# Optimization experiments

Hardware: AMD Instinct MI355X
Metric: run time of the kernel (lower is better)

The kernel has to match this reference:

```python
import jax, jax.numpy as jnp
import numpy as np

NUM_HEADS = 16

def setup_inputs() -> dict:
    key = jax.random.key(0)
    k0, k1, k2, k3 = jax.random.split(key, 4)
    B, N, Nl, Nr, D = 16, 257, 514, 512, 1024
    gather_idx = jax.random.randint(k0, (B, N), 0, B * Nl + Nr, dtype=jnp.int64 if jax.config.jax_enable_x64 else jnp.int32)
    lhs_states = jax.random.normal(k1, (4, B, Nl, D), dtype=jnp.float32)
    rhs_states = jax.random.normal(k2, (4, 1, Nr, D), dtype=jnp.float32)
    Wo = jax.random.normal(k3, (D, D), dtype=jnp.float32) * 0.02
    bo = jnp.zeros((D,), dtype=jnp.float32)
    return {"gather_idx": gather_idx, "lhs_states": lhs_states, "rhs_states": rhs_states, "Wo": Wo, "bo": bo}


def _gather_stacked_batched_states(gather_idx, lhs_states, rhs_states):
    # lhs_states: [4, B, Nl, D] cache; rhs_states: [4, 1, Nr, D]
    # torch builds batched_states [4, 1, B*Nl+Nr, D] then gathers with [4, B, N, D] idx
    S, B, Nl, D = lhs_states.shape
    Nr = rhs_states.shape[2]
    batched = jnp.concatenate(
        [lhs_states.reshape(S, B * Nl, D), rhs_states.reshape(S, Nr, D)], axis=1
    )  # [4, B*Nl+Nr, D]
    N = gather_idx.shape[1]
    gathered = jnp.take(batched, gather_idx.reshape(-1), axis=1)  # [4, B*N, D]
    return gathered.reshape(S, B, N, D)


def reference(gather_idx, lhs_states, rhs_states, Wo, bo):
    # Gather hidden/q/k/v states from the expanded cache buffer (token reuse dispatch)
    gathered = _gather_stacked_batched_states(gather_idx, lhs_states, rhs_states)
    hidden, q, k, v = gathered[0], gathered[1], gathered[2], gathered[3]
    B, N, D = hidden.shape
    H = NUM_HEADS
    hd = D // H
    scale = hd ** -0.5
    # _shape: [B, N, D] -> [B, H, N, hd]; query scaled before bmm as in torch
    qh = (q * scale).reshape(B, N, H, hd).transpose(0, 2, 1, 3)
    kh = k.reshape(B, N, H, hd).transpose(0, 2, 1, 3)
    vh = v.reshape(B, N, H, hd).transpose(0, 2, 1, 3)
    attn_weights = jax.nn.softmax(jnp.einsum('bhqd,bhkd->bhqk', qh, kh), axis=-1)
    attn_out = jnp.einsum('bhqk,bhkd->bhqd', attn_weights, vh)  # [B, H, N, hd]
    attn_out = attn_out.transpose(0, 2, 1, 3).reshape(B, N, D)
    attn_out = attn_out @ Wo.T + bo  # out_proj (torch Linear)
    return hidden + attn_out  # residual
```

## Files before the change

### kernel.cpp

```cpp
#include <hip/hip_runtime.h>
#include <hip/hip_bf16.h>

typedef __attribute__((ext_vector_type(8))) short bf16x8;
typedef __attribute__((ext_vector_type(4))) float f32x4;
typedef unsigned short u16;
typedef unsigned int u32;

#define LHS_STRIDE 8421376
#define RHS_STRIDE 524288
#define TBL_SPLIT  8224
#define AN 257
#define KSD 68
#define VSD 292
#define PSD 292

__device__ __forceinline__ const float* tbl_row(int s, int g,
    const float* __restrict__ lhs, const float* __restrict__ rhs) {
  if (g < TBL_SPLIT) return lhs + (size_t)s * LHS_STRIDE + (size_t)g * 1024;
  return rhs + (size_t)s * RHS_STRIDE + (size_t)(g - TBL_SPLIT) * 1024;
}

__device__ __forceinline__ u16 f2b(float x) {
  union { __hip_bfloat16 b; u16 u; } c;
  c.b = __float2bfloat16(x);
  return c.u;
}

__device__ __forceinline__ bf16x8 mk8(ushort4 a, ushort4 b) {
  bf16x8 r;
  r[0] = (short)a.x; r[1] = (short)a.y; r[2] = (short)a.z; r[3] = (short)a.w;
  r[4] = (short)b.x; r[5] = (short)b.y; r[6] = (short)b.z; r[7] = (short)b.w;
  return r;
}

__device__ __forceinline__ void gload16(const u16* g, u16* l) {
  __builtin_amdgcn_global_load_lds((const __attribute__((address_space(1))) void*)g,
                                   (__attribute__((address_space(3))) void*)l,
                                   16, 0, 0);
}

struct __align__(16) AttnSmem {
  int idx[260];
  u16 K[272 * KSD];
  u16 VT[64 * VSD];
  u16 P[8 * 16 * PSD];
};

__global__ __launch_bounds__(512, 1) void attn_kernel(
    const int* __restrict__ gidx, const float* __restrict__ lhs,
    const float* __restrict__ rhs, u16* __restrict__ attn_out) {
  __shared__ AttnSmem sm;
  const int bh = blockIdx.x, b = bh >> 4, h = bh & 15;
  const int t = threadIdx.x, wave = t >> 6, lane = t & 63;
  const int lg = lane >> 4, lr = lane & 15;

  {
    uint4 z = {0u, 0u, 0u, 0u};
    uint4* p = (uint4*)sm.VT;
    const int n16 = (64 * VSD + 8 * 16 * PSD) * 2 / 16;
    for (int i = t; i < n16; i += 512) p[i] = z;
  }
  for (int i = t; i < AN; i += 512) sm.idx[i] = gidx[b * AN + i];
  __syncthreads();

  {
    const int sr = t >> 4, c4 = (t & 15) * 4;
    for (int pass = 0; pass < 9; ++pass) {
      int r = pass * 32 + sr;
      if (r < AN) {
        int g = sm.idx[r];
        float4 kv = *(const float4*)(tbl_row(2, g, lhs, rhs) + h * 64 + c4);
        *(ushort4*)&sm.K[r * KSD + c4] =
            make_ushort4(f2b(kv.x), f2b(kv.y), f2b(kv.z), f2b(kv.w));
        float4 vv = *(const float4*)(tbl_row(3, g, lhs, rhs) + h * 64 + c4);
        sm.VT[(c4 + 0) * VSD + r] = f2b(vv.x);
        sm.VT[(c4 + 1) * VSD + r] = f2b(vv.y);
        sm.VT[(c4 + 2) * VSD + r] = f2b(vv.z);
        sm.VT[(c4 + 3) * VSD + r] = f2b(vv.w);
      }
    }
  }
  __syncthreads();

  u16* Pw = sm.P + wave * 16 * PSD;
  for (int rt = wave; rt < 17; rt += 8) {
    const int r0 = rt * 16;

    bf16x8 qa[2];
    {
      int qrow = r0 + lr;
      int g = sm.idx[qrow < AN ? qrow : 0];
      const float* qp = tbl_row(1, g, lhs, rhs) + h * 64 + lg * 8;
#pragma unroll
      for (int kf = 0; kf < 2; ++kf) {
        float4 v0 = *(const float4*)(qp + kf * 32);
        float4 v1 = *(const float4*)(qp + kf * 32 + 4);
        bf16x8 a;
        a[0] = (short)f2b(0.125f * v0.x); a[1] = (short)f2b(0.125f * v0.y);
        a[2] = (short)f2b(0.125f * v0.z); a[3] = (short)f2b(0.125f * v0.w);
        a[4] = (short)f2b(0.125f * v1.x); a[5] = (short)f2b(0.125f * v1.y);
        a[6] = (short)f2b(0.125f * v1.z); a[7] = (short)f2b(0.125f * v1.w);
        qa[kf] = a;
      }
    }

    f32x4 s[17];
#pragma unroll
    for (int nf = 0; nf < 17; ++nf) {
      const u16* kp = &sm.K[(nf * 16 + lr) * KSD + lg * 8];
      ushort4 x0 = *(const ushort4*)kp;
      ushort4 x1 = *(const ushort4*)(kp + 4);
      ushort4 y0 = *(const ushort4*)(kp + 32);
      ushort4 y1 = *(const ushort4*)(kp + 36);
      f32x4 acc = {0.f, 0.f, 0.f, 0.f};
      acc = __builtin_amdgcn_mfma_f32_16x16x32_bf16(qa[0], mk8(x0, x1), acc, 0, 0, 0);
      acc = __builtin_amdgcn_mfma_f32_16x16x32_bf16(qa[1], mk8(y0, y1), acc, 0, 0, 0);
      s[nf] = acc;
    }
    if (lr != 0) { s[16][0] = -1e30f; s[16][1] = -1e30f; s[16][2] = -1e30f; s[16][3] = -1e30f; }

    float inv[4];
#pragma unroll
    for (int reg = 0; reg < 4; ++reg) {
      float m = -1e30f;
#pragma unroll
      for (int nf = 0; nf < 17; ++nf) m = fmaxf(m, s[nf][reg]);
#pragma unroll
      for (int off = 1; off < 16; off <<= 1) m = fmaxf(m, __shfl_xor(m, off, 16));
      float sum = 0.f;
#pragma unroll
      for (int nf = 0; nf < 17; ++nf) {
        float w = __expf(s[nf][reg] - m);
        s[nf][reg] = w;
        sum += w;
      }
#pragma unroll
      for (int off = 1; off < 16; off <<= 1) sum += __shfl_xor(sum, off, 16);
      inv[reg] = 1.0f / sum;
    }
#pragma unroll
    for (int reg = 0; reg < 4; ++reg) {
#pragma unroll
      for (int nf = 0; nf < 17; ++nf)
        Pw[(lg * 4 + reg) * PSD + nf * 16 + lr] = f2b(s[nf][reg] * inv[reg]);
    }

    f32x4 zero = {0.f, 0.f, 0.f, 0.f};
    f32x4 o[4] = {zero, zero, zero, zero};
#pragma unroll
    for (int ks = 0; ks < 9; ++ks) {
      const u16* pp = &Pw[lr * PSD + ks * 32 + lg * 8];
      bf16x8 pa = mk8(*(const ushort4*)pp, *(const ushort4*)(pp + 4));
#pragma unroll
      for (int nd = 0; nd < 4; ++nd) {
        const u16* vp = &sm.VT[(nd * 16 + lr) * VSD + ks * 32 + lg * 8];
        bf16x8 vb = mk8(*(const ushort4*)vp, *(const ushort4*)(vp + 4));
        o[nd] = __builtin_amdgcn_mfma_f32_16x16x32_bf16(pa, vb, o[nd], 0, 0, 0);
      }
    }

#pragma unroll
    for (int nd = 0; nd < 4; ++nd)
#pragma unroll
      for (int reg = 0; reg < 4; ++reg) {
        int row = r0 + lg * 4 + reg;
        if (row < AN)
          attn_out[(size_t)(b * AN + row) * 1024 + h * 64 + nd * 16 + lr] =
              f2b(o[nd][reg]);
      }
  }
}

__global__ void cvt_wo_kernel(const float* __restrict__ w, u16* __restrict__ o) {
  int i = blockIdx.x * 256 + threadIdx.x;
  float4 v = ((const float4*)w)[i];
  ((ushort4*)o)[i] = make_ushort4(f2b(v.x), f2b(v.y), f2b(v.z), f2b(v.w));
}

__global__ __launch_bounds__(256, 1) void gemm_kernel(
    const u16* __restrict__ A, const u16* __restrict__ Bw,
    const float* __restrict__ bo, const int* __restrict__ gidx,
    const float* __restrict__ lhs, const float* __restrict__ rhs,
    float* __restrict__ out) {
  __shared__ __align__(16) u16 As[128 * 32];
  __shared__ __align__(16) u16 Bs[128 * 32];
  const int t = threadIdx.x, wave = t >> 6, lane = t & 63;
  const int lg = lane >> 4, lr = lane & 15;
  const int mt = blockIdx.x >> 3, nt = blockIdx.x & 7;
  const int m0 = mt * 128, n0 = nt * 128;
  const int wm = wave >> 1, wn = wave & 1;

  f32x4 zero = {0.f, 0.f, 0.f, 0.f};
  f32x4 acc[4][4];
#pragma unroll
  for (int i = 0; i < 4; ++i)
#pragma unroll
    for (int j = 0; j < 4; ++j) acc[i][j] = zero;

  const int srow = lane >> 2;
  const int scol = (((lane & 3) ^ ((lane >> 3) & 3))) * 8;
  const int ss = (lg ^ ((lr >> 1) & 3)) * 8;

  for (int kt = 0; kt < 32; ++kt) {
    const int k0 = kt * 32;
#pragma unroll
    for (int i = 0; i < 2; ++i) {
      int row = wave * 32 + i * 16 + srow;
      int arow = m0 + row; if (arow > 4111) arow = 4111;
      gload16(A + (size_t)arow * 1024 + k0 + scol, &As[wave * 1024 + i * 512]);
      gload16(Bw + (size_t)(n0 + row) * 1024 + k0 + scol, &Bs[wave * 1024 + i * 512]);
    }
    __syncthreads();
    bf16x8 af[4], bfr[4];
#pragma unroll
    for (int i = 0; i < 4; ++i) {
      af[i]  = *(const bf16x8*)&As[(wm * 64 + i * 16 + lr) * 32 + ss];
      bfr[i] = *(const bf16x8*)&Bs[(wn * 64 + i * 16 + lr) * 32 + ss];
    }
#pragma unroll
    for (int i = 0; i < 4; ++i)
#pragma unroll
      for (int j = 0; j < 4; ++j)
        acc[i][j] = __builtin_amdgcn_mfma_f32_16x16x32_bf16(af[i], bfr[j], acc[i][j], 0, 0, 0);
    __syncthreads();
  }

#pragma unroll
  for (int i = 0; i < 4; ++i)
#pragma unroll
    for (int j = 0; j < 4; ++j)
#pragma unroll
      for (int reg = 0; reg < 4; ++reg) {
        int row = m0 + wm * 64 + i * 16 + lg * 4 + reg;
        int col = n0 + wn * 64 + j * 16 + lr;
        if (row < 4112) {
          int g = gidx[row];
          out[(size_t)row * 1024 + col] =
              tbl_row(0, g, lhs, rhs)[col] + bo[col] + acc[i][j][reg];
        }
      }
}

extern "C" void kernel_launch(void* const* d_in, const int* in_sizes, int n_in,
                              void* d_out, int out_size, void* d_ws, size_t ws_size,
                              hipStream_t stream) {
  const int*   gidx = (const int*)d_in[0];
  const float* lhs  = (const float*)d_in[1];
  const float* rhs  = (const float*)d_in[2];
  const float* Wo   = (const float*)d_in[3];
  const float* bo   = (const float*)d_in[4];
  float* out = (float*)d_out;

  u16* attn_ws = (u16*)d_ws;
  u16* wo_bf   = attn_ws + (size_t)4112 * 1024;

  cvt_wo_kernel<<<1024, 256, 0, stream>>>(Wo, wo_bf);
  attn_kernel<<<256, 512, 0, stream>>>(gidx, lhs, rhs, attn_ws);
  gemm_kernel<<<264, 256, 0, stream>>>(attn_ws, wo_bf, bo, gidx, lhs, rhs, out);
}
```

Baseline: 262.9 us.

## Fuse Wo conversion into attention, keep P in registers, double-buffer GEMM

Folds the Wo fp32-to-bf16 conversion into the attention kernel, which saves a launch. The attention kernel now prefetches K/V/Q into registers before writing shared memory. It drops the shared P buffer and the zero-init pass: QK^T is computed transposed so softmax is done per column, and the P fragments are rebuilt with cross-lane shuffles. The last key column gets its own MFMA, and occupancy is raised to 2 blocks per CU. The GEMM gets double-buffered LDS staging so global loads overlap compute, at the cost of more registers and LDS.

After: 302.2 us. 14.9% more time.

```diff
diff --git a/kernel.cpp b/kernel.cpp
--- a/kernel.cpp
+++ b/kernel.cpp
@@ -11,8 +11,7 @@
 #define TBL_SPLIT  8224
 #define AN 257
 #define KSD 68
-#define VSD 292
-#define PSD 292
+#define VSD 260
 
 __device__ __forceinline__ const float* tbl_row(int s, int g,
     const float* __restrict__ lhs, const float* __restrict__ rhs) {
@@ -24,6 +23,10 @@
   union { __hip_bfloat16 b; u16 u; } c;
   c.b = __float2bfloat16(x);
   return c.u;
+}
+
+__device__ __forceinline__ u32 pk2(float a, float b) {
+  return (u32)f2b(a) | ((u32)f2b(b) << 16);
 }
 
 __device__ __forceinline__ bf16x8 mk8(ushort4 a, ushort4 b) {
@@ -40,56 +43,39 @@
 }
 
 struct __align__(16) AttnSmem {
-  int idx[260];
   u16 K[272 * KSD];
   u16 VT[64 * VSD];
-  u16 P[8 * 16 * PSD];
 };
 
-__global__ __launch_bounds__(512, 1) void attn_kernel(
+__global__ __launch_bounds__(512, 2) void attn_kernel(
     const int* __restrict__ gidx, const float* __restrict__ lhs,
-    const float* __restrict__ rhs, u16* __restrict__ attn_out) {
+    const float* __restrict__ rhs, u16* __restrict__ attn_out,
+    const float* __restrict__ Wo, u16* __restrict__ wo_bf) {
   __shared__ AttnSmem sm;
   const int bh = blockIdx.x, b = bh >> 4, h = bh & 15;
   const int t = threadIdx.x, wave = t >> 6, lane = t & 63;
   const int lg = lane >> 4, lr = lane & 15;
-
-  {
-    uint4 z = {0u, 0u, 0u, 0u};
-    uint4* p = (uint4*)sm.VT;
-    const int n16 = (64 * VSD + 8 * 16 * PSD) * 2 / 16;
-    for (int i = t; i < n16; i += 512) p[i] = z;
-  }
-  for (int i = t; i < AN; i += 512) sm.idx[i] = gidx[b * AN + i];
-  __syncthreads();
-
-  {
-    const int sr = t >> 4, c4 = (t & 15) * 4;
-    for (int pass = 0; pass < 9; ++pass) {
-      int r = pass * 32 + sr;
-      if (r < AN) {
-        int g = sm.idx[r];
-        float4 kv = *(const float4*)(tbl_row(2, g, lhs, rhs) + h * 64 + c4);
-        *(ushort4*)&sm.K[r * KSD + c4] =
-            make_ushort4(f2b(kv.x), f2b(kv.y), f2b(kv.z), f2b(kv.w));
-        float4 vv = *(const float4*)(tbl_row(3, g, lhs, rhs) + h * 64 + c4);
-        sm.VT[(c4 + 0) * VSD + r] = f2b(vv.x);
-        sm.VT[(c4 + 1) * VSD + r] = f2b(vv.y);
-        sm.VT[(c4 + 2) * VSD + r] = f2b(vv.z);
-        sm.VT[(c4 + 3) * VSD + r] = f2b(vv.w);
-      }
-    }
-  }
-  __syncthreads();
-
-  u16* Pw = sm.P + wave * 16 * PSD;
-  for (int rt = wave; rt < 17; rt += 8) {
-    const int r0 = rt * 16;
-
-    bf16x8 qa[2];
-    {
-      int qrow = r0 + lr;
-      int g = sm.idx[qrow < AN ? qrow : 0];
+  const int* gi = gidx + b * AN;
+
+  const int sr = t >> 4, c4v = (t & 15) * 4;
+  float4 kreg[9], vreg[9];
+#pragma unroll
+  for (int p = 0; p < 9; ++p) {
+    int r = p * 32 + sr;
+    int rc = (r < AN) ? r : 0;
+    int g = gi[rc];
+    kreg[p] = *(const float4*)(tbl_row(2, g, lhs, rhs) + h * 64 + c4v);
+    vreg[p] = *(const float4*)(tbl_row(3, g, lhs, rhs) + h * 64 + c4v);
+  }
+
+  const int ntile = (wave == 0) ? 3 : 2;
+  const int rts[3] = {wave, wave + 8, 16};
+  bf16x8 qa[3][2];
+#pragma unroll
+  for (int ti = 0; ti < 3; ++ti) {
+    if (ti < ntile) {
+      int qrow = rts[ti] * 16 + lr; if (qrow > 256) qrow = 256;
+      int g = gi[qrow];
       const float* qp = tbl_row(1, g, lhs, rhs) + h * 64 + lg * 8;
 #pragma unroll
       for (int kf = 0; kf < 2; ++kf) {
@@ -100,9 +86,42 @@
         a[2] = (short)f2b(0.125f * v0.z); a[3] = (short)f2b(0.125f * v0.w);
         a[4] = (short)f2b(0.125f * v1.x); a[5] = (short)f2b(0.125f * v1.y);
         a[6] = (short)f2b(0.125f * v1.z); a[7] = (short)f2b(0.125f * v1.w);
-        qa[kf] = a;
-      }
-    }
+        qa[ti][kf] = a;
+      }
+    }
+  }
+
+  {
+    const float4* src = (const float4*)Wo;
+    ushort4* dst = (ushort4*)wo_bf;
+    int i0 = bh * 1024 + t * 2;
+#pragma unroll
+    for (int u = 0; u < 2; ++u) {
+      float4 v = src[i0 + u];
+      dst[i0 + u] = make_ushort4(f2b(v.x), f2b(v.y), f2b(v.z), f2b(v.w));
+    }
+  }
+
+#pragma unroll
+  for (int p = 0; p < 9; ++p) {
+    int r = p * 32 + sr;
+    if (r < AN) {
+      *(ushort4*)&sm.K[r * KSD + c4v] =
+          make_ushort4(f2b(kreg[p].x), f2b(kreg[p].y), f2b(kreg[p].z), f2b(kreg[p].w));
+      sm.VT[(c4v + 0) * VSD + r] = f2b(vreg[p].x);
+      sm.VT[(c4v + 1) * VSD + r] = f2b(vreg[p].y);
+      sm.VT[(c4v + 2) * VSD + r] = f2b(vreg[p].z);
+      sm.VT[(c4v + 3) * VSD + r] = f2b(vreg[p].w);
+    }
+  }
+  __syncthreads();
+
+  const int srcE = lr + ((lane & 16) << 1);
+  const int srcO = srcE + 16;
+  const bool useE = (lg < 2);
+
+  for (int ti = 0; ti < ntile; ++ti) {
+    const int r0 = rts[ti] * 16;
 
     f32x4 s[17];
 #pragma unroll
@@ -113,49 +132,65 @@
       ushort4 y0 = *(const ushort4*)(kp + 32);
       ushort4 y1 = *(const ushort4*)(kp + 36);
       f32x4 acc = {0.f, 0.f, 0.f, 0.f};
-      acc = __builtin_amdgcn_mfma_f32_16x16x32_bf16(qa[0], mk8(x0, x1), acc, 0, 0, 0);
-      acc = __builtin_amdgcn_mfma_f32_16x16x32_bf16(qa[1], mk8(y0, y1), acc, 0, 0, 0);
+      acc = __builtin_amdgcn_mfma_f32_16x16x32_bf16(mk8(x0, x1), qa[ti][0], acc, 0, 0, 0);
+      acc = __builtin_amdgcn_mfma_f32_16x16x32_bf16(mk8(y0, y1), qa[ti][1], acc, 0, 0, 0);
       s[nf] = acc;
     }
-    if (lr != 0) { s[16][0] = -1e30f; s[16][1] = -1e30f; s[16][2] = -1e30f; s[16][3] = -1e30f; }
-
-    float inv[4];
-#pragma unroll
-    for (int reg = 0; reg < 4; ++reg) {
-      float m = -1e30f;
-#pragma unroll
-      for (int nf = 0; nf < 17; ++nf) m = fmaxf(m, s[nf][reg]);
-#pragma unroll
-      for (int off = 1; off < 16; off <<= 1) m = fmaxf(m, __shfl_xor(m, off, 16));
-      float sum = 0.f;
-#pragma unroll
-      for (int nf = 0; nf < 17; ++nf) {
-        float w = __expf(s[nf][reg] - m);
-        s[nf][reg] = w;
+    s[16][1] = -1e30f; s[16][2] = -1e30f; s[16][3] = -1e30f;
+    if (lg != 0) s[16][0] = -1e30f;
+
+    float m = -1e30f;
+#pragma unroll
+    for (int nf = 0; nf < 17; ++nf)
+      m = fmaxf(m, fmaxf(fmaxf(s[nf][0], s[nf][1]), fmaxf(s[nf][2], s[nf][3])));
+    m = fmaxf(m, __shfl_xor(m, 16));
+    m = fmaxf(m, __shfl_xor(m, 32));
+    float sum = 0.f;
+#pragma unroll
+    for (int nf = 0; nf < 17; ++nf) {
+#pragma unroll
+      for (int r = 0; r < 4; ++r) {
+        float w = __expf(s[nf][r] - m);
+        s[nf][r] = w;
         sum += w;
       }
-#pragma unroll
-      for (int off = 1; off < 16; off <<= 1) sum += __shfl_xor(sum, off, 16);
-      inv[reg] = 1.0f / sum;
-    }
-#pragma unroll
-    for (int reg = 0; reg < 4; ++reg) {
-#pragma unroll
-      for (int nf = 0; nf < 17; ++nf)
-        Pw[(lg * 4 + reg) * PSD + nf * 16 + lr] = f2b(s[nf][reg] * inv[reg]);
-    }
+    }
+    sum += __shfl_xor(sum, 16);
+    sum += __shfl_xor(sum, 32);
+    const float inv = 1.0f / sum;
 
     f32x4 zero = {0.f, 0.f, 0.f, 0.f};
     f32x4 o[4] = {zero, zero, zero, zero};
 #pragma unroll
-    for (int ks = 0; ks < 9; ++ks) {
-      const u16* pp = &Pw[lr * PSD + ks * 32 + lg * 8];
-      bf16x8 pa = mk8(*(const ushort4*)pp, *(const ushort4*)(pp + 4));
+    for (int ks = 0; ks < 8; ++ks) {
+      u32 e0 = pk2(s[2 * ks][0] * inv, s[2 * ks][1] * inv);
+      u32 e1 = pk2(s[2 * ks][2] * inv, s[2 * ks][3] * inv);
+      u32 f0 = pk2(s[2 * ks + 1][0] * inv, s[2 * ks + 1][1] * inv);
+      u32 f1 = pk2(s[2 * ks + 1][2] * inv, s[2 * ks + 1][3] * inv);
+      u32 A0 = (u32)__shfl((int)e0, srcE), A1 = (u32)__shfl((int)e1, srcE);
+      u32 A2 = (u32)__shfl((int)e0, srcO), A3 = (u32)__shfl((int)e1, srcO);
+      u32 B0 = (u32)__shfl((int)f0, srcE), B1 = (u32)__shfl((int)f1, srcE);
+      u32 B2 = (u32)__shfl((int)f0, srcO), B3 = (u32)__shfl((int)f1, srcO);
+      union { u32 w[4]; bf16x8 v; } pa;
+      pa.w[0] = useE ? A0 : B0; pa.w[1] = useE ? A1 : B1;
+      pa.w[2] = useE ? A2 : B2; pa.w[3] = useE ? A3 : B3;
 #pragma unroll
       for (int nd = 0; nd < 4; ++nd) {
         const u16* vp = &sm.VT[(nd * 16 + lr) * VSD + ks * 32 + lg * 8];
         bf16x8 vb = mk8(*(const ushort4*)vp, *(const ushort4*)(vp + 4));
-        o[nd] = __builtin_amdgcn_mfma_f32_16x16x32_bf16(pa, vb, o[nd], 0, 0, 0);
+        o[nd] = __builtin_amdgcn_mfma_f32_16x16x32_bf16(pa.v, vb, o[nd], 0, 0, 0);
+      }
+    }
+    {
+      union { u32 w[4]; bf16x8 v; } pa;
+      pa.w[0] = pk2(s[16][0] * inv, 0.f);
+      pa.w[1] = 0; pa.w[2] = 0; pa.w[3] = 0;
+#pragma unroll
+      for (int nd = 0; nd < 4; ++nd) {
+        union { u32 w[4]; bf16x8 v; } vb;
+        vb.w[0] = (lg == 0) ? (u32)sm.VT[(nd * 16 + lr) * VSD + 256] : 0u;
+        vb.w[1] = 0; vb.w[2] = 0; vb.w[3] = 0;
+        o[nd] = __builtin_amdgcn_mfma_f32_16x16x32_bf16(pa.v, vb.v, o[nd], 0, 0, 0);
       }
     }
 
@@ -171,19 +206,13 @@
   }
 }
 
-__global__ void cvt_wo_kernel(const float* __restrict__ w, u16* __restrict__ o) {
-  int i = blockIdx.x * 256 + threadIdx.x;
-  float4 v = ((const float4*)w)[i];
-  ((ushort4*)o)[i] = make_ushort4(f2b(v.x), f2b(v.y), f2b(v.z), f2b(v.w));
-}
-
 __global__ __launch_bounds__(256, 1) void gemm_kernel(
     const u16* __restrict__ A, const u16* __restrict__ Bw,
     const float* __restrict__ bo, const int* __restrict__ gidx,
     const float* __restrict__ lhs, const float* __restrict__ rhs,
     float* __restrict__ out) {
-  __shared__ __align__(16) u16 As[128 * 32];
-  __shared__ __align__(16) u16 Bs[128 * 32];
+  __shared__ __align__(16) u16 As[2][128 * 32];
+  __shared__ __align__(16) u16 Bs[2][128 * 32];
   const int t = threadIdx.x, wave = t >> 6, lane = t & 63;
   const int lg = lane >> 4, lr = lane & 15;
   const int mt = blockIdx.x >> 3, nt = blockIdx.x & 7;
@@ -201,21 +230,28 @@
   const int scol = (((lane & 3) ^ ((lane >> 3) & 3))) * 8;
   const int ss = (lg ^ ((lr >> 1) & 3)) * 8;
 
+#define STAGE(buf, kt)                                                          \
+  {                                                                             \
+    const int k0 = (kt) * 32;                                                   \
+    _Pragma("unroll")                                                           \
+    for (int i = 0; i < 2; ++i) {                                               \
+      int row = wave * 32 + i * 16 + srow;                                      \
+      int arow = m0 + row; if (arow > 4111) arow = 4111;                        \
+      gload16(A + (size_t)arow * 1024 + k0 + scol, &As[buf][wave * 1024 + i * 512]); \
+      gload16(Bw + (size_t)(n0 + row) * 1024 + k0 + scol, &Bs[buf][wave * 1024 + i * 512]); \
+    }                                                                           \
+  }
+
+  STAGE(0, 0)
+  __syncthreads();
+  int cur = 0;
   for (int kt = 0; kt < 32; ++kt) {
-    const int k0 = kt * 32;
-#pragma unroll
-    for (int i = 0; i < 2; ++i) {
-      int row = wave * 32 + i * 16 + srow;
-      int arow = m0 + row; if (arow > 4111) arow = 4111;
-      gload16(A + (size_t)arow * 1024 + k0 + scol, &As[wave * 1024 + i * 512]);
-      gload16(Bw + (size_t)(n0 + row) * 1024 + k0 + scol, &Bs[wave * 1024 + i * 512]);
-    }
-    __syncthreads();
+    if (kt < 31) STAGE(cur ^ 1, kt + 1)
     bf16x8 af[4], bfr[4];
 #pragma unroll
     for (int i = 0; i < 4; ++i) {
-      af[i]  = *(const bf16x8*)&As[(wm * 64 + i * 16 + lr) * 32 + ss];
-      bfr[i] = *(const bf16x8*)&Bs[(wn * 64 + i * 16 + lr) * 32 + ss];
+      af[i]  = *(const bf16x8*)&As[cur][(wm * 64 + i * 16 + lr) * 32 + ss];
+      bfr[i] = *(const bf16x8*)&Bs[cur][(wn * 64 + i * 16 + lr) * 32 + ss];
     }
 #pragma unroll
     for (int i = 0; i < 4; ++i)
@@ -223,7 +259,9 @@
       for (int j = 0; j < 4; ++j)
         acc[i][j] = __builtin_amdgcn_mfma_f32_16x16x32_bf16(af[i], bfr[j], acc[i][j], 0, 0, 0);
     __syncthreads();
-  }
+    cur ^= 1;
+  }
+#undef STAGE
 
 #pragma unroll
   for (int i = 0; i < 4; ++i)
@@ -254,7 +292,6 @@
   u16* attn_ws = (u16*)d_ws;
   u16* wo_bf   = attn_ws + (size_t)4112 * 1024;
 
-  cvt_wo_kernel<<<1024, 256, 0, stream>>>(Wo, wo_bf);
-  attn_kernel<<<256, 512, 0, stream>>>(gidx, lhs, rhs, attn_ws);
+  attn_kernel<<<256, 512, 0, stream>>>(gidx, lhs, rhs, attn_ws, Wo, wo_bf);
   gemm_kernel<<<264, 256, 0, stream>>>(attn_ws, wo_bf, bo, gidx, lhs, rhs, out);
 }
```
